# Optimization experiments

Measured on AMD Instinct MI355X. Metric: run time of the kernel, lower is better.

## Reference

```python
import jax, jax.numpy as jnp
import numpy as np

N = 10000   # num_nodes
F = 64      # latent_dim
U = 128     # num_units
B = 8       # batch
K = 2       # gcn_step
E = 160000  # edges (avg degree 16)
M = 2 * K + 1  # num_matrices = len(supports)*gcn_step + 1


def setup_inputs() -> dict:
    rng = np.random.default_rng(0)
    rows = rng.integers(0, N, E).astype(np.int32)
    cols = rng.integers(0, N, E).astype(np.int32)
    vals = (rng.random(E).astype(np.float32) + 0.1)
    # random-walk normalization D^{-1} A, per the original utils.calculate_random_walk_matrix
    deg_out = np.zeros(N, np.float32); np.add.at(deg_out, rows, vals)
    deg_in = np.zeros(N, np.float32); np.add.at(deg_in, cols, vals)
    # support1 = (D_out^{-1} A)^T : out[c] += vals/d_out[r] * x[r]  -> dst=cols, src=rows
    w1 = vals / np.maximum(deg_out[rows], 1e-8)
    # support2 = (D_in^{-1} A^T)^T : out[r] += vals/d_in[c] * x[c]  -> dst=rows, src=cols
    w2 = vals / np.maximum(deg_in[cols], 1e-8)

    key = jax.random.key(0)
    ks = jax.random.split(key, 4)

    def xavier(k, shape):
        std = (2.0 / (shape[0] + shape[1])) ** 0.5
        return jax.random.normal(k, shape, jnp.float32) * std

    return {
        'y': jax.random.normal(ks[0], (B, N * F), jnp.float32),
        'W_lat': xavier(ks[1], (M * F, F)),
        'b_lat': jnp.ones((F,), jnp.float32),   # bias_start=1.0, shared (keyed by length)
        'W_units': xavier(ks[2], (M * F, U)),
        'b_units': jnp.zeros((U,), jnp.float32),
        'W_final': xavier(ks[3], (M * U, F)),
        'sup1_w': jnp.asarray(w1),
        'sup2_w': jnp.asarray(w2),
        'edge_rows': jnp.asarray(rows),
        'edge_cols': jnp.asarray(cols),
    }


def _spmm(dst, src, w, x):
    # sparse matmul S @ x with S given as COO edge list; x: (N, Fin, B)
    return jax.ops.segment_sum(w[:, None, None] * x[src], dst, num_segments=N)


def _gconv(x, supports, W, b):
    # x: (B, N, Fin) -> (B, N*Fout); Chebyshev diffusion convolution
    Bsz, n, fin = x.shape
    x0 = jnp.transpose(x, (1, 2, 0))  # (N, Fin, B)
    xs = [x0]
    for dst, src, w in supports:
        xk_2 = x0
        x1 = _spmm(dst, src, w, x0)
        xs.append(x1)
        for _ in range(2, K + 1):
            x2 = 2.0 * _spmm(dst, src, w, x1) - xk_2
            xs.append(x2)
            xk_2, x1 = x1, x2
    X = jnp.stack(xs, axis=-1)                       # (N, Fin, B, M)
    X = jnp.transpose(X, (2, 0, 1, 3)).reshape(Bsz * n, fin * len(xs))  # feature-major, matrix-minor
    out = X @ W + b
    return out.reshape(Bsz, n * W.shape[1])


def reference(y, W_lat, b_lat, W_units, b_units, W_final, sup1_w, sup2_w, edge_rows, edge_cols):
    supports = [(edge_cols, edge_rows, sup1_w), (edge_rows, edge_cols, sup2_w)]
    x = y.reshape(B, N, F)
    # theta gate (bias_start=1.0 via shared b_lat)
    theta = jax.nn.sigmoid(_gconv(x, supports, W_lat, b_lat))
    # ode_func_net: gen_layers=1 hidden gconv + final gconv (final bias is shared b_lat!)
    c = jnp.tanh(_gconv(x, supports, W_units, b_units)).reshape(B, N, U)
    c = jnp.tanh(_gconv(c, supports, W_final, b_lat))
    return -theta * c
```

## Files before the change

kernel.cpp:

```cpp
#include <hip/hip_runtime.h>

#define N_NODES 10000
#define NEDGE 160000
#define NB 80000
#define SCAN_CH 40

typedef unsigned int u32;
typedef unsigned short u16;
typedef __attribute__((ext_vector_type(8))) short short8;
typedef __attribute__((ext_vector_type(4))) float float4v;

__device__ __forceinline__ float bf2f(u16 h) { return __uint_as_float(((u32)h) << 16); }
__device__ __forceinline__ u16 f2bf(float f) {
    u32 u = __float_as_uint(f);
    return (u16)((u + 0x7fffu + ((u >> 16) & 1u)) >> 16);
}
__device__ __forceinline__ float lo16(u32 u) { return __uint_as_float(u << 16); }
__device__ __forceinline__ float hi16(u32 u) { return __uint_as_float(u & 0xffff0000u); }
__device__ __forceinline__ u32 pack2(float a, float b) {
    return (u32)f2bf(a) | (((u32)f2bf(b)) << 16);
}
__device__ __forceinline__ float fast_tanh(float v) {
    return 1.f - 2.f / (__expf(2.f * v) + 1.f);
}

__device__ __forceinline__ void bpack_body(const float* __restrict__ W, u16* __restrict__ out,
                                           int FIN, int NOUT, int idx) {
    int j = idx & 7;
    int lane = (idx >> 3) & 63;
    int rest = idx >> 9;
    int CT = NOUT >> 4;
    int ct = rest % CT;
    int ks = rest / CT;
    int k = ks * 32 + (lane >> 4) * 8 + j;
    int col = ct * 16 + (lane & 15);
    int wrow = (k % FIN) * 5 + (k / FIN);
    out[idx] = f2bf(W[wrow * NOUT + col]);
}

__global__ __launch_bounds__(256) void prep_kernel(
    const float2* __restrict__ y, u32* __restrict__ X0,
    const float* __restrict__ W_lat, u16* __restrict__ bpk1,
    const float* __restrict__ W_units, u16* __restrict__ bpk2,
    const float* __restrict__ W_final, u16* __restrict__ bpkP,
    int* __restrict__ cnt) {
    int b = blockIdx.x, t = threadIdx.x;
    if (b < 10000) {
        int idx = b * 256 + t;
        int fh = idx & 31;
        int rb = idx >> 5;
        int bb = rb & 7;
        int n = rb >> 3;
        float2 v = y[((size_t)bb * N_NODES + n) * 32 + fh];
        X0[idx] = pack2(v.x, v.y);
    } else if (b < 10080) {
        bpack_body(W_lat, bpk1, 64, 64, (b - 10000) * 256 + t);
    } else if (b < 10240) {
        bpack_body(W_units, bpk2, 64, 128, (b - 10080) * 256 + t);
    } else if (b < 10400) {
        int idx = (b - 10240) * 256 + t;
        int j8 = idx & 7;
        int lane = (idx >> 3) & 63;
        int rest = idx >> 9;
        int ct = rest % 20;
        int ks = rest / 20;
        int k = ks * 32 + (lane >> 4) * 8 + j8;
        int col = ct * 16 + (lane & 15);
        int slot = col >> 6, j = col & 63;
        float v;
        if (slot == 0)
            v = W_final[(k * 5 + 0) * 64 + j] - W_final[(k * 5 + 2) * 64 + j] -
                W_final[(k * 5 + 4) * 64 + j];
        else
            v = W_final[(k * 5 + slot) * 64 + j];
        bpkP[idx] = f2bf(v);
    } else {
        int idx = (b - 10400) * 256 + t;
        if (idx < 2 * N_NODES) cnt[idx] = 0;
    }
}

__global__ void count_kernel(const int* __restrict__ rows, const int* __restrict__ cols,
                             int* __restrict__ cnt1, int* __restrict__ cnt2) {
    int e = blockIdx.x * 256 + threadIdx.x;
    if (e < NEDGE) {
        atomicAdd(&cnt1[cols[e]], 1);
        atomicAdd(&cnt2[rows[e]], 1);
    }
}

__global__ void blocksum_kernel(const int* __restrict__ cnt, int* __restrict__ bsums) {
    __shared__ int red[4];
    int arr = blockIdx.x / SCAN_CH;
    int c = blockIdx.x % SCAN_CH;
    int idx = c * 256 + threadIdx.x;
    int v = (idx < N_NODES) ? cnt[arr * N_NODES + idx] : 0;
#pragma unroll
    for (int off = 32; off; off >>= 1) v += __shfl_down(v, off, 64);
    int wv = threadIdx.x >> 6, ln = threadIdx.x & 63;
    if (ln == 0) red[wv] = v;
    __syncthreads();
    if (threadIdx.x == 0) bsums[blockIdx.x] = red[0] + red[1] + red[2] + red[3];
}

__global__ void scanmid_kernel(int* __restrict__ bsums, int* __restrict__ rowptr1,
                               int* __restrict__ rowptr2) {
    __shared__ int lds[128];
    int t = threadIdx.x;
    int seg = t >> 6, pos = t & 63;
    int v = (pos < SCAN_CH) ? bsums[seg * SCAN_CH + pos] : 0;
    lds[t] = v;
    __syncthreads();
    for (int off = 1; off < 64; off <<= 1) {
        int add = (pos >= off) ? lds[t - off] : 0;
        __syncthreads();
        lds[t] += add;
        __syncthreads();
    }
    if (pos < SCAN_CH) bsums[seg * SCAN_CH + pos] = pos ? lds[t - 1] : 0;
    if (t == 0) { rowptr1[N_NODES] = NEDGE; rowptr2[N_NODES] = NEDGE; }
}

__global__ void scanapply_kernel(int* __restrict__ cnt, const int* __restrict__ bsums,
                                 int* __restrict__ rowptr1, int* __restrict__ rowptr2) {
    __shared__ int lds[256];
    int arr = blockIdx.x / SCAN_CH;
    int c = blockIdx.x % SCAN_CH;
    int idx = c * 256 + threadIdx.x;
    bool ok = idx < N_NODES;
    int v = ok ? cnt[arr * N_NODES + idx] : 0;
    int t = threadIdx.x;
    lds[t] = v;
    __syncthreads();
    for (int off = 1; off < 256; off <<= 1) {
        int add = (t >= off) ? lds[t - off] : 0;
        __syncthreads();
        lds[t] += add;
        __syncthreads();
    }
    int excl = lds[t] - v + bsums[blockIdx.x];
    if (ok) {
        int* rp = arr ? rowptr2 : rowptr1;
        rp[idx] = excl;
        cnt[arr * N_NODES + idx] = excl;
    }
}

__global__ void scatter_kernel(const int* __restrict__ rows, const int* __restrict__ cols,
                               const float* __restrict__ w1, const float* __restrict__ w2,
                               int* __restrict__ cur1, int* __restrict__ cur2,
                               int2* __restrict__ edges1, int2* __restrict__ edges2) {
    int e = blockIdx.x * 256 + threadIdx.x;
    if (e < NEDGE) {
        int r = rows[e], c = cols[e];
        int p1 = atomicAdd(&cur1[c], 1);
        edges1[p1] = make_int2(r, __float_as_int(w1[e]));
        int p2 = atomicAdd(&cur2[r], 1);
        edges2[p2] = make_int2(c, __float_as_int(w2[e]));
    }
}

__device__ __forceinline__ void gather_row(const u32* __restrict__ Xin,
                                           const int* __restrict__ rp,
                                           const int2* __restrict__ eg,
                                           int n, int lane, float* acc) {
    int e0 = rp[n], e1 = rp[n + 1];
    for (int base = e0; base < e1; base += 64) {
        int m = min(64, e1 - base);
        int2 me = make_int2(0, 0);
        if (lane < m) me = eg[base + lane];
        for (int j = 0; j < m; j++) {
            int src = __shfl(me.x, j, 64);
            float w = __int_as_float(__shfl(me.y, j, 64));
            uint4 u = *(const uint4*)(Xin + (size_t)src * 256 + lane * 4);
            acc[0] += w * lo16(u.x); acc[1] += w * hi16(u.x);
            acc[2] += w * lo16(u.y); acc[3] += w * hi16(u.y);
            acc[4] += w * lo16(u.z); acc[5] += w * hi16(u.z);
            acc[6] += w * lo16(u.w); acc[7] += w * hi16(u.w);
        }
    }
}

__global__ __launch_bounds__(256) void spmm2_kernel(
    const u32* __restrict__ XinA, const u32* __restrict__ XprevA, u32* __restrict__ XoutA,
    const u32* __restrict__ XinB, const u32* __restrict__ XprevB, u32* __restrict__ XoutB,
    const int* __restrict__ rowptr1, const int2* __restrict__ edges1,
    const int* __restrict__ rowptr2, const int2* __restrict__ edges2,
    float alpha, float beta) {
    int lane = threadIdx.x & 63;
    int v = blockIdx.x * 4 + (threadIdx.x >> 6);
    if (v >= 2 * N_NODES) return;
    bool hB = v >= N_NODES;
    int n = hB ? v - N_NODES : v;
    const u32* Xin = hB ? XinB : XinA;
    const u32* Xprev = hB ? XprevB : XprevA;
    u32* Xout = hB ? XoutB : XoutA;
    const int* rp = hB ? rowptr2 : rowptr1;
    const int2* eg = hB ? edges2 : edges1;

    float acc[8] = {0.f, 0.f, 0.f, 0.f, 0.f, 0.f, 0.f, 0.f};
    gather_row(Xin, rp, eg, n, lane, acc);

    size_t o = (size_t)n * 256 + lane * 4;
    if (beta != 0.f) {
        uint4 p = *(const uint4*)(Xprev + o);
        acc[0] = alpha * acc[0] + beta * lo16(p.x); acc[1] = alpha * acc[1] + beta * hi16(p.x);
        acc[2] = alpha * acc[2] + beta * lo16(p.y); acc[3] = alpha * acc[3] + beta * hi16(p.y);
        acc[4] = alpha * acc[4] + beta * lo16(p.z); acc[5] = alpha * acc[5] + beta * hi16(p.z);
        acc[6] = alpha * acc[6] + beta * lo16(p.w); acc[7] = alpha * acc[7] + beta * hi16(p.w);
    } else {
#pragma unroll
        for (int i = 0; i < 8; i++) acc[i] *= alpha;
    }
    uint4 r;
    r.x = pack2(acc[0], acc[1]);
    r.y = pack2(acc[2], acc[3]);
    r.z = pack2(acc[4], acc[5]);
    r.w = pack2(acc[6], acc[7]);
    *(uint4*)(Xout + o) = r;
}

__global__ __launch_bounds__(256) void spmm_final_kernel(
    const u32* __restrict__ T1, const u32* __restrict__ T2,
    const u32* __restrict__ Q, const u32* __restrict__ theta,
    const int* __restrict__ rowptr1, const int2* __restrict__ edges1,
    const int* __restrict__ rowptr2, const int2* __restrict__ edges2,
    float* __restrict__ outF) {
    int lane = threadIdx.x & 63;
    int n = blockIdx.x * 4 + (threadIdx.x >> 6);
    if (n >= N_NODES) return;

    float acc[8] = {0.f, 0.f, 0.f, 0.f, 0.f, 0.f, 0.f, 0.f};
    gather_row(T1, rowptr1, edges1, n, lane, acc);
    gather_row(T2, rowptr2, edges2, n, lane, acc);

    size_t o = (size_t)n * 256 + lane * 4;
    uint4 q = *(const uint4*)(Q + o);
    uint4 th = *(const uint4*)(theta + o);
    float res[8];
    res[0] = -lo16(th.x) * fast_tanh(lo16(q.x) + acc[0]);
    res[1] = -hi16(th.x) * fast_tanh(hi16(q.x) + acc[1]);
    res[2] = -lo16(th.y) * fast_tanh(lo16(q.y) + acc[2]);
    res[3] = -hi16(th.y) * fast_tanh(hi16(q.y) + acc[3]);
    res[4] = -lo16(th.z) * fast_tanh(lo16(q.z) + acc[4]);
    res[5] = -hi16(th.z) * fast_tanh(hi16(q.z) + acc[5]);
    res[6] = -lo16(th.w) * fast_tanh(lo16(q.w) + acc[6]);
    res[7] = -hi16(th.w) * fast_tanh(hi16(q.w) + acc[7]);
    int b = lane >> 3;
    int f0 = ((lane * 4) & 31) * 2;
    float* dst = outF + (size_t)b * (N_NODES * 64) + (size_t)n * 64 + f0;
    *(float4*)(dst) = make_float4(res[0], res[1], res[2], res[3]);
    *(float4*)(dst + 4) = make_float4(res[4], res[5], res[6], res[7]);
}

struct Slabs { const u16* p[5]; };

template <int FIN, int NM, int NOUT, int ACT>
__global__ __launch_bounds__(256) void gemm_kernel(
    Slabs A, const u16* __restrict__ Bp, const float* __restrict__ bias,
    u16* __restrict__ Cout) {
    constexpr int K = NM * FIN;
    constexpr int KS = K / 32;
    constexpr int CT = NOUT / 16;
    int lane = threadIdx.x & 63;
    int wave = threadIdx.x >> 6;
    int rowBase = blockIdx.x * 128 + wave * 32;
    int mrow = lane & 15;
    int kq = lane >> 4;

    float4v acc[2][CT];
#pragma unroll
    for (int s = 0; s < 2; s++)
#pragma unroll
        for (int c = 0; c < CT; c++) acc[s][c] = (float4v){0.f, 0.f, 0.f, 0.f};

    for (int ks = 0; ks < KS; ks++) {
        int k = ks * 32 + kq * 8;
        int m = k / FIN;
        int koff = k % FIN;
        const u16* abase = A.p[m] + (size_t)(rowBase + mrow) * FIN + koff;
        short8 a0 = *(const short8*)(abase);
        short8 a1 = *(const short8*)(abase + 16 * FIN);
        const u16* bbase = Bp + ((size_t)(ks * CT) * 64 + lane) * 8;
#pragma unroll
        for (int ct = 0; ct < CT; ct++) {
            short8 b = *(const short8*)(bbase + (size_t)ct * 64 * 8);
            acc[0][ct] = __builtin_amdgcn_mfma_f32_16x16x32_bf16(a0, b, acc[0][ct], 0, 0, 0);
            acc[1][ct] = __builtin_amdgcn_mfma_f32_16x16x32_bf16(a1, b, acc[1][ct], 0, 0, 0);
        }
    }

#pragma unroll
    for (int sub = 0; sub < 2; sub++) {
        int rowq = rowBase + sub * 16 + kq * 4;
#pragma unroll
        for (int ct = 0; ct < CT; ct++) {
            int col = ct * 16 + mrow;
            float bsv;
            if (ACT == 0) bsv = (col < 64) ? bias[col] : 0.f;
            else bsv = bias[col];
#pragma unroll
            for (int i = 0; i < 4; i++) {
                float v = acc[sub][ct][i] + bsv;
                int r = rowq + i;
                if (ACT == 0) {
                    Cout[(size_t)(col >> 6) * ((size_t)NB * 64) + (size_t)r * 64 + (col & 63)] = f2bf(v);
                } else if (ACT == 1) {
                    v = 1.f / (1.f + __expf(-v));
                    Cout[(size_t)r * NOUT + col] = f2bf(v);
                } else {
                    Cout[(size_t)r * NOUT + col] = f2bf(fast_tanh(v));
                }
            }
        }
    }
}

extern "C" void kernel_launch(void* const* d_in, const int* in_sizes, int n_in,
                              void* d_out, int out_size, void* d_ws, size_t ws_size,
                              hipStream_t stream) {
    const float* y     = (const float*)d_in[0];
    const float* W_lat = (const float*)d_in[1];
    const float* b_lat = (const float*)d_in[2];
    const float* W_units = (const float*)d_in[3];
    const float* b_units = (const float*)d_in[4];
    const float* W_final = (const float*)d_in[5];
    const float* sup1w = (const float*)d_in[6];
    const float* sup2w = (const float*)d_in[7];
    const int* rows    = (const int*)d_in[8];
    const int* cols    = (const int*)d_in[9];
    float* out = (float*)d_out;

    char* ws = (char*)d_ws;
    size_t off = 0;
    auto alloc = [&](size_t bytes) -> void* {
        void* p = ws + off;
        off += (bytes + 511) & ~(size_t)511;
        return p;
    };
    int* rowptr1 = (int*)alloc((N_NODES + 1) * 4);
    int* rowptr2 = (int*)alloc((N_NODES + 1) * 4);
    int* cnt = (int*)alloc((size_t)2 * N_NODES * 4);
    int* cnt1 = cnt;
    int* cnt2 = cnt + N_NODES;
    int* bsums = (int*)alloc(2 * SCAN_CH * 4);
    int2* edges1 = (int2*)alloc((size_t)NEDGE * 8);
    int2* edges2 = (int2*)alloc((size_t)NEDGE * 8);
    u16* bpk1 = (u16*)alloc((size_t)320 * 64 * 2);
    u16* bpk2 = (u16*)alloc((size_t)320 * 128 * 2);
    u16* bpkP = (u16*)alloc((size_t)40960 * 2);
    u16* theta = (u16*)alloc((size_t)NB * 64 * 2);
    u16* S = (u16*)alloc((size_t)5 * NB * 64 * 2);
    u16* H0 = (u16*)alloc((size_t)NB * 128 * 2);
    u16* T1 = (u16*)alloc((size_t)NB * 64 * 2);
    u16* T2 = (u16*)alloc((size_t)NB * 64 * 2);
    u16* P = S;

    const size_t SLAB = (size_t)NB * 64;

    prep_kernel<<<10479, 256, 0, stream>>>((const float2*)y, (u32*)S, W_lat, bpk1,
                                           W_units, bpk2, W_final, bpkP, cnt);
    count_kernel<<<(NEDGE + 255) / 256, 256, 0, stream>>>(rows, cols, cnt1, cnt2);
    blocksum_kernel<<<2 * SCAN_CH, 256, 0, stream>>>(cnt, bsums);
    scanmid_kernel<<<1, 128, 0, stream>>>(bsums, rowptr1, rowptr2);
    scanapply_kernel<<<2 * SCAN_CH, 256, 0, stream>>>(cnt, bsums, rowptr1, rowptr2);
    scatter_kernel<<<(NEDGE + 255) / 256, 256, 0, stream>>>(rows, cols, sup1w, sup2w,
                                                            cnt1, cnt2, edges1, edges2);

    const u32* S0 = (const u32*)S;
    u32* X1 = (u32*)(S + 1 * SLAB);
    u32* X2 = (u32*)(S + 2 * SLAB);
    u32* X3 = (u32*)(S + 3 * SLAB);
    u32* X4 = (u32*)(S + 4 * SLAB);
    spmm2_kernel<<<5000, 256, 0, stream>>>(S0, nullptr, X1, S0, nullptr, X3,
                                           rowptr1, edges1, rowptr2, edges2, 1.f, 0.f);
    spmm2_kernel<<<5000, 256, 0, stream>>>(X1, S0, X2, X3, S0, X4,
                                           rowptr1, edges1, rowptr2, edges2, 2.f, -1.f);

    Slabs SX;
    for (int m = 0; m < 5; m++) SX.p[m] = S + (size_t)m * SLAB;
    gemm_kernel<64, 5, 64, 1><<<625, 256, 0, stream>>>(SX, bpk1, b_lat, theta);
    gemm_kernel<64, 5, 128, 2><<<625, 256, 0, stream>>>(SX, bpk2, b_units, H0);

    Slabs SH;
    SH.p[0] = H0;
    gemm_kernel<128, 1, 320, 0><<<625, 256, 0, stream>>>(SH, bpkP, b_lat, P);

    const u32* Q  = (const u32*)(P + 0 * SLAB);
    const u32* P1 = (const u32*)(P + 1 * SLAB);
    const u32* P2 = (const u32*)(P + 2 * SLAB);
    const u32* P3 = (const u32*)(P + 3 * SLAB);
    const u32* P4 = (const u32*)(P + 4 * SLAB);
    spmm2_kernel<<<5000, 256, 0, stream>>>(P2, (const u32*)P1, (u32*)T1,
                                           P4, (const u32*)P3, (u32*)T2,
                                           rowptr1, edges1, rowptr2, edges2, 2.f, 1.f);
    spmm_final_kernel<<<2500, 256, 0, stream>>>((const u32*)T1, (const u32*)T2, Q,
                                                (const u32*)theta,
                                                rowptr1, edges1, rowptr2, edges2, out);
}
```

Baseline: 385.4 us.

## Fuse theta and hidden-unit GEMMs into one 192-column GEMM with preloaded A

Merges the W_lat and W_units weight packing into a single 192-column packed matrix and runs one GEMM producing both the sigmoid theta output and the tanh hidden output. The A operand (five stacked slabs) is then read from global memory once instead of twice. All A fragments for the whole K dimension are also preloaded into registers before the MFMA loop. This raises register pressure (24 accumulator tiles for two sub-rows plus 20 A fragments), which may cut occupancy or cause spills.

Measured after the change: 377.5 us. 2.1% less time.

```diff
diff --git a/kernel.cpp b/kernel.cpp
--- a/kernel.cpp
+++ b/kernel.cpp
@@ -24,24 +24,10 @@
     return 1.f - 2.f / (__expf(2.f * v) + 1.f);
 }
 
-__device__ __forceinline__ void bpack_body(const float* __restrict__ W, u16* __restrict__ out,
-                                           int FIN, int NOUT, int idx) {
-    int j = idx & 7;
-    int lane = (idx >> 3) & 63;
-    int rest = idx >> 9;
-    int CT = NOUT >> 4;
-    int ct = rest % CT;
-    int ks = rest / CT;
-    int k = ks * 32 + (lane >> 4) * 8 + j;
-    int col = ct * 16 + (lane & 15);
-    int wrow = (k % FIN) * 5 + (k / FIN);
-    out[idx] = f2bf(W[wrow * NOUT + col]);
-}
-
 __global__ __launch_bounds__(256) void prep_kernel(
     const float2* __restrict__ y, u32* __restrict__ X0,
-    const float* __restrict__ W_lat, u16* __restrict__ bpk1,
-    const float* __restrict__ W_units, u16* __restrict__ bpk2,
+    const float* __restrict__ W_lat, const float* __restrict__ W_units,
+    u16* __restrict__ bpk12,
     const float* __restrict__ W_final, u16* __restrict__ bpkP,
     int* __restrict__ cnt) {
     int b = blockIdx.x, t = threadIdx.x;
@@ -53,10 +39,18 @@
         int n = rb >> 3;
         float2 v = y[((size_t)bb * N_NODES + n) * 32 + fh];
         X0[idx] = pack2(v.x, v.y);
-    } else if (b < 10080) {
-        bpack_body(W_lat, bpk1, 64, 64, (b - 10000) * 256 + t);
     } else if (b < 10240) {
-        bpack_body(W_units, bpk2, 64, 128, (b - 10080) * 256 + t);
+        int idx = (b - 10000) * 256 + t;
+        int j = idx & 7;
+        int lane = (idx >> 3) & 63;
+        int rest = idx >> 9;
+        int ct = rest % 12;
+        int ks = rest / 12;
+        int k = ks * 32 + (lane >> 4) * 8 + j;
+        int col = ct * 16 + (lane & 15);
+        int wrow = (k % 64) * 5 + (k / 64);
+        float v = (col < 64) ? W_lat[wrow * 64 + col] : W_units[wrow * 128 + (col - 64)];
+        bpk12[idx] = f2bf(v);
     } else if (b < 10400) {
         int idx = (b - 10240) * 256 + t;
         int j8 = idx & 7;
@@ -255,10 +249,10 @@
 
 struct Slabs { const u16* p[5]; };
 
-template <int FIN, int NM, int NOUT, int ACT>
+template <int FIN, int NM, int NOUT, int MODE>
 __global__ __launch_bounds__(256) void gemm_kernel(
-    Slabs A, const u16* __restrict__ Bp, const float* __restrict__ bias,
-    u16* __restrict__ Cout) {
+    Slabs A, const u16* __restrict__ Bp, const float* __restrict__ bias1,
+    const float* __restrict__ bias2, u16* __restrict__ O1, u16* __restrict__ O2) {
     constexpr int K = NM * FIN;
     constexpr int KS = K / 32;
     constexpr int CT = NOUT / 16;
@@ -268,25 +262,31 @@
     int mrow = lane & 15;
     int kq = lane >> 4;
 
-    float4v acc[2][CT];
-#pragma unroll
-    for (int s = 0; s < 2; s++)
-#pragma unroll
-        for (int c = 0; c < CT; c++) acc[s][c] = (float4v){0.f, 0.f, 0.f, 0.f};
-
+    short8 a0[KS], a1[KS];
+#pragma unroll
     for (int ks = 0; ks < KS; ks++) {
         int k = ks * 32 + kq * 8;
         int m = k / FIN;
         int koff = k % FIN;
         const u16* abase = A.p[m] + (size_t)(rowBase + mrow) * FIN + koff;
-        short8 a0 = *(const short8*)(abase);
-        short8 a1 = *(const short8*)(abase + 16 * FIN);
+        a0[ks] = *(const short8*)(abase);
+        a1[ks] = *(const short8*)(abase + 16 * FIN);
+    }
+
+    float4v acc[2][CT];
+#pragma unroll
+    for (int s = 0; s < 2; s++)
+#pragma unroll
+        for (int c = 0; c < CT; c++) acc[s][c] = (float4v){0.f, 0.f, 0.f, 0.f};
+
+#pragma unroll
+    for (int ks = 0; ks < KS; ks++) {
         const u16* bbase = Bp + ((size_t)(ks * CT) * 64 + lane) * 8;
 #pragma unroll
         for (int ct = 0; ct < CT; ct++) {
             short8 b = *(const short8*)(bbase + (size_t)ct * 64 * 8);
-            acc[0][ct] = __builtin_amdgcn_mfma_f32_16x16x32_bf16(a0, b, acc[0][ct], 0, 0, 0);
-            acc[1][ct] = __builtin_amdgcn_mfma_f32_16x16x32_bf16(a1, b, acc[1][ct], 0, 0, 0);
+            acc[0][ct] = __builtin_amdgcn_mfma_f32_16x16x32_bf16(a0[ks], b, acc[0][ct], 0, 0, 0);
+            acc[1][ct] = __builtin_amdgcn_mfma_f32_16x16x32_bf16(a1[ks], b, acc[1][ct], 0, 0, 0);
         }
     }
 
@@ -297,19 +297,21 @@
         for (int ct = 0; ct < CT; ct++) {
             int col = ct * 16 + mrow;
             float bsv;
-            if (ACT == 0) bsv = (col < 64) ? bias[col] : 0.f;
-            else bsv = bias[col];
+            if (MODE == 0) bsv = (col < 64) ? bias1[col] : 0.f;
+            else bsv = (col < 64) ? bias1[col] : bias2[col - 64];
 #pragma unroll
             for (int i = 0; i < 4; i++) {
                 float v = acc[sub][ct][i] + bsv;
                 int r = rowq + i;
-                if (ACT == 0) {
-                    Cout[(size_t)(col >> 6) * ((size_t)NB * 64) + (size_t)r * 64 + (col & 63)] = f2bf(v);
-                } else if (ACT == 1) {
-                    v = 1.f / (1.f + __expf(-v));
-                    Cout[(size_t)r * NOUT + col] = f2bf(v);
+                if (MODE == 0) {
+                    O1[(size_t)(col >> 6) * ((size_t)NB * 64) + (size_t)r * 64 + (col & 63)] = f2bf(v);
                 } else {
-                    Cout[(size_t)r * NOUT + col] = f2bf(fast_tanh(v));
+                    if (col < 64) {
+                        v = 1.f / (1.f + __expf(-v));
+                        O1[(size_t)r * 64 + col] = f2bf(v);
+                    } else {
+                        O2[(size_t)r * 128 + (col - 64)] = f2bf(fast_tanh(v));
+                    }
                 }
             }
         }
@@ -346,8 +348,7 @@
     int* bsums = (int*)alloc(2 * SCAN_CH * 4);
     int2* edges1 = (int2*)alloc((size_t)NEDGE * 8);
     int2* edges2 = (int2*)alloc((size_t)NEDGE * 8);
-    u16* bpk1 = (u16*)alloc((size_t)320 * 64 * 2);
-    u16* bpk2 = (u16*)alloc((size_t)320 * 128 * 2);
+    u16* bpk12 = (u16*)alloc((size_t)61440 * 2);
     u16* bpkP = (u16*)alloc((size_t)40960 * 2);
     u16* theta = (u16*)alloc((size_t)NB * 64 * 2);
     u16* S = (u16*)alloc((size_t)5 * NB * 64 * 2);
@@ -358,8 +359,8 @@
 
     const size_t SLAB = (size_t)NB * 64;
 
-    prep_kernel<<<10479, 256, 0, stream>>>((const float2*)y, (u32*)S, W_lat, bpk1,
-                                           W_units, bpk2, W_final, bpkP, cnt);
+    prep_kernel<<<10479, 256, 0, stream>>>((const float2*)y, (u32*)S, W_lat, W_units,
+                                           bpk12, W_final, bpkP, cnt);
     count_kernel<<<(NEDGE + 255) / 256, 256, 0, stream>>>(rows, cols, cnt1, cnt2);
     blocksum_kernel<<<2 * SCAN_CH, 256, 0, stream>>>(cnt, bsums);
     scanmid_kernel<<<1, 128, 0, stream>>>(bsums, rowptr1, rowptr2);
@@ -379,12 +380,11 @@
 
     Slabs SX;
     for (int m = 0; m < 5; m++) SX.p[m] = S + (size_t)m * SLAB;
-    gemm_kernel<64, 5, 64, 1><<<625, 256, 0, stream>>>(SX, bpk1, b_lat, theta);
-    gemm_kernel<64, 5, 128, 2><<<625, 256, 0, stream>>>(SX, bpk2, b_units, H0);
+    gemm_kernel<64, 5, 192, 1><<<625, 256, 0, stream>>>(SX, bpk12, b_lat, b_units, theta, H0);
 
     Slabs SH;
     SH.p[0] = H0;
-    gemm_kernel<128, 1, 320, 0><<<625, 256, 0, stream>>>(SH, bpkP, b_lat, P);
+    gemm_kernel<128, 1, 320, 0><<<625, 256, 0, stream>>>(SH, bpkP, b_lat, nullptr, P, nullptr);
 
     const u32* Q  = (const u32*)(P + 0 * SLAB);
     const u32* P1 = (const u32*)(P + 1 * SLAB);
```
